# Kernel optimization log

Hardware: AMD Instinct MI355X
Metric: run time of the kernel (lower is better)

## Reference

```python
import jax, jax.numpy as jnp
import numpy as np

KERNEL_SIZE = 5
SIGMA = 2.0
HALF_K = KERNEL_SIZE // 2


def _gaussian_kernel():
    # torch: arange(-k//2+1, k//2+1) with python floor div -> [-2,...,2] for k=5
    ax = jnp.arange(-(KERNEL_SIZE // 2), KERNEL_SIZE // 2 + 1, dtype=jnp.float32)
    xx, yy = jnp.meshgrid(ax, ax, indexing='ij')
    k = jnp.exp(-(xx ** 2 + yy ** 2) / (2.0 * SIGMA ** 2))
    return k / k.sum()  # [5,5]


def setup_inputs() -> dict:
    key = jax.random.key(0)
    k1, k2 = jax.random.split(key)
    feature_map = jax.random.normal(k1, (512, 256, 256), dtype=jnp.float32)
    keypoints = jax.random.randint(k2, (4096, 2), 0, 256, dtype=jnp.int64)
    return {"feature_map": feature_map, "keypoints": keypoints}


def reference(feature_map, keypoints):
    C, H, W = feature_map.shape
    kern = _gaussian_kernel().astype(feature_map.dtype)  # [5,5]
    x = jnp.clip(keypoints[:, 0].astype(jnp.int32), HALF_K, W - HALF_K - 1)  # [N]
    y = jnp.clip(keypoints[:, 1].astype(jnp.int32), HALF_K, H - HALF_K - 1)  # [N]

    def pool_one(xi, yi):
        patch = jax.lax.dynamic_slice(
            feature_map, (0, yi - HALF_K, xi - HALF_K), (C, KERNEL_SIZE, KERNEL_SIZE)
        )  # [C,5,5]
        return jnp.einsum('chw,hw->c', patch, kern)  # [C]

    return jax.vmap(pool_one)(x, y)  # [N,C]
```

## Files before the change

kernel.cpp:

```cpp
#include <hip/hip_runtime.h>


#define NC  512
#define NH  256
#define NW  256
#define NKP 4096

#define NSTRIP 8
#define STRIP_SHIFT 5
#define SLICE_ROWS 36
#define STR 260

#define WS_LIST_OFF_I 8192

__global__ __launch_bounds__(1024) void bucket_kernel(
    const int* __restrict__ kp, unsigned* __restrict__ ws_i, int n_kp)
{
    __shared__ int hist[NSTRIP];
    const int t = threadIdx.x;

    if (t < NSTRIP) hist[t] = 0;
    __syncthreads();

    int      q[4], lr[4];
    unsigned pk[4];
    bool     valid[4];
#pragma unroll
    for (int j = 0; j < 4; ++j) {
        const int i = t + j * 1024;
        valid[j] = (i < n_kp);
        q[j] = 0; lr[j] = 0; pk[j] = 0u;
        if (valid[j]) {
            int x = kp[2 * i + 0];
            int y = kp[2 * i + 1];
            x = min(max(x, 2), NW - 3);
            y = min(max(y, 2), NH - 3);
            q[j]  = y >> STRIP_SHIFT;
            lr[j] = atomicAdd(&hist[q[j]], 1);
            pk[j] = (unsigned)i | ((unsigned)x << 12) | ((unsigned)y << 20);
        }
    }
    __syncthreads();

    if (t < NSTRIP) ws_i[t] = (unsigned)hist[t];

#pragma unroll
    for (int j = 0; j < 4; ++j)
        if (valid[j])
            ws_i[WS_LIST_OFF_I + q[j] * NKP + lr[j]] = pk[j];
}

__global__ __launch_bounds__(256) void pool_kernel(
    const float* __restrict__ fm, const unsigned* __restrict__ ws_i,
    float* __restrict__ out)
{
    __shared__ float plane[SLICE_ROWS * STR];

    const int b     = blockIdx.x;
    const int x7    = b & 7;
    const int inner = b >> 3;
    const int hi    = inner >> 7;
    const int rem   = inner & 127;
    const int q     = rem >> 4;
    const int l16   = rem & 15;
    const int chunk = (hi << 3) | x7;
    const int c     = (chunk << 4) | l16;

    const int t    = threadIdx.x;
    const int w    = t >> 6;
    const int lane = t & 63;
    const int ybase = (q << STRIP_SHIFT) - 2;

    const int cnt = (int)ws_i[q];

    const float* src = fm + ((size_t)c << 16);
#pragma unroll
    for (int it = 0; it < 9; ++it) {
        const int row = w + (it << 2);
        const int gr  = ybase + row;
        if ((unsigned)gr < 256u) {
            const float* g = src + ((size_t)gr << 8) + (lane << 2);
            float*       l = &plane[row * STR + (lane << 2)];
            __builtin_amdgcn_global_load_lds(
                (const __attribute__((address_space(1))) void*)g,
                (__attribute__((address_space(3))) void*)l,
                16, 0, 0);
        }
    }

    const float e1 = 0.8824969025845955f;
    const float e2 = 0.6065306597126334f;
    const float s  = 2.0f * (e1 + e2) + 1.0f;
    const float inv_s2 = 1.0f / (s * s);
    const float g[5] = {e2, e1, 1.0f, e1, e2};
    float gy[5];
#pragma unroll
    for (int i = 0; i < 5; i++) gy[i] = g[i] * inv_s2;

    const unsigned* list = ws_i + WS_LIST_OFF_I + q * NKP;

    unsigned pk = (t < cnt) ? list[t] : 0u;

    __syncthreads();

    for (int e = t; e < cnt; e += 256) {
        const int n  = (int)(pk & 0xFFFu);
        const int xc = (int)((pk >> 12) & 0xFFu);
        const int yc = (int)((pk >> 20) & 0xFFu);

        if (e + 256 < cnt) pk = list[e + 256];

        const int x0 = xc - 2;
        const int r  = x0 & 3;
        const int xa = x0 - r;
        float wx[8];
#pragma unroll
        for (int i = 0; i < 8; i++)
            wx[i] = (i >= r && i < r + 5) ? g[i - r] : 0.0f;

        const int lr0 = yc - (q << STRIP_SHIFT);
        float acc = 0.0f;
#pragma unroll
        for (int dy = 0; dy < 5; dy++) {
            const float* rowp = &plane[(lr0 + dy) * STR + xa];
            float4 a  = *(const float4*)rowp;
            float4 b4 = *(const float4*)(rowp + 4);
            acc += gy[dy] * (a.x * wx[0] + a.y * wx[1] + a.z * wx[2] + a.w * wx[3]
                           + b4.x * wx[4] + b4.y * wx[5] + b4.z * wx[6] + b4.w * wx[7]);
        }
        out[(size_t)n * NC + c] = acc;
    }
}

__global__ __launch_bounds__(256) void gpool_direct_kernel(
    const float* __restrict__ fm, const int* __restrict__ kp,
    float* __restrict__ out)
{
    const int n = blockIdx.x;
    const int t = threadIdx.x;

    int x = kp[2 * n + 0];
    int y = kp[2 * n + 1];
    x = min(max(x, 2), NW - 3);
    y = min(max(y, 2), NH - 3);

    const float e1 = 0.8824969025845955f;
    const float e2 = 0.6065306597126334f;
    const float s  = 2.0f * (e1 + e2) + 1.0f;
    const float inv_s2 = 1.0f / (s * s);
    float g[5] = {e2, e1, 1.0f, e1, e2};
    float gy[5];
#pragma unroll
    for (int i = 0; i < 5; i++) gy[i] = g[i] * inv_s2;

    const int x0 = x - 2;
    const int r  = x0 & 3;
    const int xa = x0 - r;
    float wx[8];
#pragma unroll
    for (int i = 0; i < 8; i++)
        wx[i] = (i >= r && i < r + 5) ? g[i - r] : 0.0f;

    const float* base0 = fm + ((size_t)t * NH + (y - 2)) * NW + xa;
    const float* base1 = fm + ((size_t)(t + 256) * NH + (y - 2)) * NW + xa;

    float acc0 = 0.0f, acc1 = 0.0f;
#pragma unroll
    for (int dy = 0; dy < 5; dy++) {
        const float4* p0 = (const float4*)(base0 + dy * NW);
        const float4* p1 = (const float4*)(base1 + dy * NW);
        float4 a0 = p0[0], b0 = p0[1], a1 = p1[0], b1 = p1[1];
        acc0 += gy[dy] * (a0.x * wx[0] + a0.y * wx[1] + a0.z * wx[2] + a0.w * wx[3]
                        + b0.x * wx[4] + b0.y * wx[5] + b0.z * wx[6] + b0.w * wx[7]);
        acc1 += gy[dy] * (a1.x * wx[0] + a1.y * wx[1] + a1.z * wx[2] + a1.w * wx[3]
                        + b1.x * wx[4] + b1.y * wx[5] + b1.z * wx[6] + b1.w * wx[7]);
    }

    out[(size_t)n * NC + t]       = acc0;
    out[(size_t)n * NC + t + 256] = acc1;
}

extern "C" void kernel_launch(void* const* d_in, const int* in_sizes, int n_in,
                              void* d_out, int out_size, void* d_ws, size_t ws_size,
                              hipStream_t stream)
{
    const float* fm  = (const float*)d_in[0];
    const int*   kp  = (const int*)d_in[1];
    float*       out = (float*)d_out;
    const int n_kp   = in_sizes[1] / 2;

    const size_t need = (WS_LIST_OFF_I + (size_t)NSTRIP * NKP) * sizeof(unsigned);
    if (ws_size >= need && n_kp == NKP) {
        unsigned* ws_i = (unsigned*)d_ws;

        bucket_kernel<<<1, 1024, 0, stream>>>(kp, ws_i, n_kp);

        pool_kernel<<<NC * NSTRIP, 256, 0, stream>>>(fm, ws_i, out);
    } else {
        gpool_direct_kernel<<<n_kp, 256, 0, stream>>>(fm, kp, out);
    }
}
```

Measured before the change: 200.7 us.

## Fuse keypoint bucketing into pool kernel via per-block wave-ballot compaction

Drops the separate single-block bucket kernel and its global workspace lists. Each pool block now reads all keypoints itself and compacts the ones in its row strip into an LDS list using per-wave ballot and popcount, with a capped list and an overflow path that rescans. This removes a serial launch and the dependency on a one-block kernel, at the cost of every one of the 4096 blocks redundantly reading and filtering all keypoints.

After: 199.0 us. Within noise of the previous version (-0.8%).

```diff
diff --git a/kernel.cpp b/kernel.cpp
--- a/kernel.cpp
+++ b/kernel.cpp
@@ -10,51 +10,15 @@
 #define STRIP_SHIFT 5
 #define SLICE_ROWS 36
 #define STR 260
-
-#define WS_LIST_OFF_I 8192
-
-__global__ __launch_bounds__(1024) void bucket_kernel(
-    const int* __restrict__ kp, unsigned* __restrict__ ws_i, int n_kp)
-{
-    __shared__ int hist[NSTRIP];
-    const int t = threadIdx.x;
-
-    if (t < NSTRIP) hist[t] = 0;
-    __syncthreads();
-
-    int      q[4], lr[4];
-    unsigned pk[4];
-    bool     valid[4];
-#pragma unroll
-    for (int j = 0; j < 4; ++j) {
-        const int i = t + j * 1024;
-        valid[j] = (i < n_kp);
-        q[j] = 0; lr[j] = 0; pk[j] = 0u;
-        if (valid[j]) {
-            int x = kp[2 * i + 0];
-            int y = kp[2 * i + 1];
-            x = min(max(x, 2), NW - 3);
-            y = min(max(y, 2), NH - 3);
-            q[j]  = y >> STRIP_SHIFT;
-            lr[j] = atomicAdd(&hist[q[j]], 1);
-            pk[j] = (unsigned)i | ((unsigned)x << 12) | ((unsigned)y << 20);
-        }
-    }
-    __syncthreads();
-
-    if (t < NSTRIP) ws_i[t] = (unsigned)hist[t];
-
-#pragma unroll
-    for (int j = 0; j < 4; ++j)
-        if (valid[j])
-            ws_i[WS_LIST_OFF_I + q[j] * NKP + lr[j]] = pk[j];
-}
+#define CAPW 192
 
 __global__ __launch_bounds__(256) void pool_kernel(
-    const float* __restrict__ fm, const unsigned* __restrict__ ws_i,
+    const float* __restrict__ fm, const int* __restrict__ kp,
     float* __restrict__ out)
 {
-    __shared__ float plane[SLICE_ROWS * STR];
+    __shared__ float    plane[SLICE_ROWS * STR];
+    __shared__ unsigned lds_list[4 * CAPW];
+    __shared__ int      cnt[4];
 
     const int b     = blockIdx.x;
     const int x7    = b & 7;
@@ -70,8 +34,13 @@
     const int w    = t >> 6;
     const int lane = t & 63;
     const int ybase = (q << STRIP_SHIFT) - 2;
-
-    const int cnt = (int)ws_i[q];
+    const unsigned long long lmlt = (1ull << lane) - 1ull;
+
+    const int4* kp4 = (const int4*)kp;
+    int4 vv[8];
+#pragma unroll
+    for (int it = 0; it < 8; ++it)
+        vv[it] = kp4[(w << 9) + (it << 6) + lane];
 
     const float* src = fm + ((size_t)c << 16);
 #pragma unroll
@@ -79,14 +48,43 @@
         const int row = w + (it << 2);
         const int gr  = ybase + row;
         if ((unsigned)gr < 256u) {
-            const float* g = src + ((size_t)gr << 8) + (lane << 2);
-            float*       l = &plane[row * STR + (lane << 2)];
+            const float* gp = src + ((size_t)gr << 8) + (lane << 2);
+            float*       lp = &plane[row * STR + (lane << 2)];
             __builtin_amdgcn_global_load_lds(
-                (const __attribute__((address_space(1))) void*)g,
-                (__attribute__((address_space(3))) void*)l,
+                (const __attribute__((address_space(1))) void*)gp,
+                (__attribute__((address_space(3))) void*)lp,
                 16, 0, 0);
         }
     }
+
+    int off = 0;
+#pragma unroll
+    for (int it = 0; it < 8; ++it) {
+        const int i0 = (((w << 9) + (it << 6) + lane) << 1);
+        {
+            const int x = min(max(vv[it].x, 2), NW - 3);
+            const int y = min(max(vv[it].y, 2), NH - 3);
+            const bool m = ((y >> STRIP_SHIFT) == q);
+            const unsigned long long bal = __ballot(m);
+            const int pos = off + __popcll(bal & lmlt);
+            if (m && pos < CAPW)
+                lds_list[w * CAPW + pos] =
+                    (unsigned)i0 | ((unsigned)x << 12) | ((unsigned)y << 20);
+            off += __popcll(bal);
+        }
+        {
+            const int x = min(max(vv[it].z, 2), NW - 3);
+            const int y = min(max(vv[it].w, 2), NH - 3);
+            const bool m = ((y >> STRIP_SHIFT) == q);
+            const unsigned long long bal = __ballot(m);
+            const int pos = off + __popcll(bal & lmlt);
+            if (m && pos < CAPW)
+                lds_list[w * CAPW + pos] =
+                    (unsigned)(i0 + 1) | ((unsigned)x << 12) | ((unsigned)y << 20);
+            off += __popcll(bal);
+        }
+    }
+    if (lane == 0) cnt[w] = off;
 
     const float e1 = 0.8824969025845955f;
     const float e2 = 0.6065306597126334f;
@@ -97,38 +95,76 @@
 #pragma unroll
     for (int i = 0; i < 5; i++) gy[i] = g[i] * inv_s2;
 
-    const unsigned* list = ws_i + WS_LIST_OFF_I + q * NKP;
-
-    unsigned pk = (t < cnt) ? list[t] : 0u;
-
     __syncthreads();
 
-    for (int e = t; e < cnt; e += 256) {
-        const int n  = (int)(pk & 0xFFFu);
-        const int xc = (int)((pk >> 12) & 0xFFu);
-        const int yc = (int)((pk >> 20) & 0xFFu);
-
-        if (e + 256 < cnt) pk = list[e + 256];
-
-        const int x0 = xc - 2;
-        const int r  = x0 & 3;
-        const int xa = x0 - r;
-        float wx[8];
-#pragma unroll
-        for (int i = 0; i < 8; i++)
-            wx[i] = (i >= r && i < r + 5) ? g[i - r] : 0.0f;
-
-        const int lr0 = yc - (q << STRIP_SHIFT);
-        float acc = 0.0f;
-#pragma unroll
-        for (int dy = 0; dy < 5; dy++) {
-            const float* rowp = &plane[(lr0 + dy) * STR + xa];
-            float4 a  = *(const float4*)rowp;
-            float4 b4 = *(const float4*)(rowp + 4);
-            acc += gy[dy] * (a.x * wx[0] + a.y * wx[1] + a.z * wx[2] + a.w * wx[3]
-                           + b4.x * wx[4] + b4.y * wx[5] + b4.z * wx[6] + b4.w * wx[7]);
-        }
-        out[(size_t)n * NC + c] = acc;
+    for (int seg = 0; seg < 4; ++seg) {
+        const int cs = min(cnt[seg], CAPW);
+        for (int e = t; e < cs; e += 256) {
+            const unsigned pk = lds_list[seg * CAPW + e];
+            const int n  = (int)(pk & 0xFFFu);
+            const int xc = (int)((pk >> 12) & 0xFFu);
+            const int yc = (int)((pk >> 20) & 0xFFu);
+
+            const int x0 = xc - 2;
+            const int r  = x0 & 3;
+            const int xa = x0 - r;
+            float wx[8];
+#pragma unroll
+            for (int i = 0; i < 8; i++)
+                wx[i] = (i >= r && i < r + 5) ? g[i - r] : 0.0f;
+
+            const int lr0 = yc - (q << STRIP_SHIFT);
+            float acc = 0.0f;
+#pragma unroll
+            for (int dy = 0; dy < 5; dy++) {
+                const float* rowp = &plane[(lr0 + dy) * STR + xa];
+                float4 a  = *(const float4*)rowp;
+                float4 b4 = *(const float4*)(rowp + 4);
+                acc += gy[dy] * (a.x * wx[0] + a.y * wx[1] + a.z * wx[2] + a.w * wx[3]
+                               + b4.x * wx[4] + b4.y * wx[5] + b4.z * wx[6] + b4.w * wx[7]);
+            }
+            out[(size_t)n * NC + c] = acc;
+        }
+    }
+
+    if (cnt[w] > CAPW) {
+        int off2 = 0;
+#pragma unroll 1
+        for (int it = 0; it < 8; ++it) {
+            const int4 v = kp4[(w << 9) + (it << 6) + lane];
+            const int i0 = (((w << 9) + (it << 6) + lane) << 1);
+#pragma unroll
+            for (int half = 0; half < 2; ++half) {
+                const int xr = half ? v.z : v.x;
+                const int yr = half ? v.w : v.y;
+                const int x = min(max(xr, 2), NW - 3);
+                const int y = min(max(yr, 2), NH - 3);
+                const bool m = ((y >> STRIP_SHIFT) == q);
+                const unsigned long long bal = __ballot(m);
+                const int pos = off2 + __popcll(bal & lmlt);
+                if (m && pos >= CAPW) {
+                    const int x0 = x - 2;
+                    const int r  = x0 & 3;
+                    const int xa = x0 - r;
+                    float wx[8];
+#pragma unroll
+                    for (int i = 0; i < 8; i++)
+                        wx[i] = (i >= r && i < r + 5) ? g[i - r] : 0.0f;
+                    const int lr0 = y - (q << STRIP_SHIFT);
+                    float acc = 0.0f;
+#pragma unroll
+                    for (int dy = 0; dy < 5; dy++) {
+                        const float* rowp = &plane[(lr0 + dy) * STR + xa];
+                        float4 a  = *(const float4*)rowp;
+                        float4 b4 = *(const float4*)(rowp + 4);
+                        acc += gy[dy] * (a.x * wx[0] + a.y * wx[1] + a.z * wx[2] + a.w * wx[3]
+                                       + b4.x * wx[4] + b4.y * wx[5] + b4.z * wx[6] + b4.w * wx[7]);
+                    }
+                    out[(size_t)(i0 + half) * NC + c] = acc;
+                }
+                off2 += __popcll(bal);
+            }
+        }
     }
 }
 
@@ -189,13 +225,10 @@
     float*       out = (float*)d_out;
     const int n_kp   = in_sizes[1] / 2;
 
-    const size_t need = (WS_LIST_OFF_I + (size_t)NSTRIP * NKP) * sizeof(unsigned);
-    if (ws_size >= need && n_kp == NKP) {
-        unsigned* ws_i = (unsigned*)d_ws;
-
-        bucket_kernel<<<1, 1024, 0, stream>>>(kp, ws_i, n_kp);
-
-        pool_kernel<<<NC * NSTRIP, 256, 0, stream>>>(fm, ws_i, out);
+    (void)d_ws; (void)ws_size;
+
+    if (n_kp == NKP) {
+        pool_kernel<<<NC * NSTRIP, 256, 0, stream>>>(fm, kp, out);
     } else {
         gpool_direct_kernel<<<n_kp, 256, 0, stream>>>(fm, kp, out);
     }
```
